# Optimization experiments

Measured on AMD Instinct MI355X. Metric: run time of the kernel, lower is better.

Reference implementation:

```python
import jax, jax.numpy as jnp
import numpy as np

B, S, H = 4, 1024, 1024
NH, HD = 16, 64
SCALE = 1.0 / np.sqrt(HD)
VERB_BIAS, ROOT_BIAS, SUFFIX_BIAS = 2.0, 1.5, 1.2
BIG = np.float32(1e9)


def setup_inputs() -> dict:
    key = jax.random.key(0)
    ks = jax.random.split(key, 10)
    inp = {
        "hidden_states": jax.random.normal(ks[0], (B, S, H), dtype=jnp.float32),
        "morpho_types": jax.random.randint(ks[1], (B, S), 0, 5, dtype=jnp.int32),
        # torch Linear: y = x @ W.T + b; store W already transposed as [in, out]
        "Wq": jax.random.normal(ks[2], (H, H), dtype=jnp.float32) * 0.02,
        "bq": jnp.zeros((H,), dtype=jnp.float32),
        "Wk": jax.random.normal(ks[3], (H, H), dtype=jnp.float32) * 0.02,
        "bk": jnp.zeros((H,), dtype=jnp.float32),
        "Wv": jax.random.normal(ks[4], (H, H), dtype=jnp.float32) * 0.02,
        "bv": jnp.zeros((H,), dtype=jnp.float32),
        "Wo": jax.random.normal(ks[5], (H, H), dtype=jnp.float32) * 0.02,
        "bo": jnp.zeros((H,), dtype=jnp.float32),
    }
    return inp


def _morpho_bias(morpho_types):
    """Vectorized equivalent of _create_morpho_bias_mask. Returns [B, S, S]
    (the torch version broadcasts the same bias over all heads)."""
    is_verb = morpho_types == 2                      # [B, S]
    pos = jnp.arange(S)
    dist = jnp.abs(pos[:, None] - pos[None, :])      # [S, S]
    # mask non-verb columns with a huge distance; argmin ties -> smallest j,
    # matching torch's argmin over ascending verb_positions
    dist_m = jnp.where(is_verb[:, None, :], dist[None], BIG)  # [B, S, S]
    nearest = jnp.argmin(dist_m, axis=-1)            # [B, S]
    has_verb = jnp.any(is_verb, axis=-1)             # [B]
    verb_term = VERB_BIAS * jax.nn.one_hot(nearest, S, dtype=jnp.float32)
    verb_term = verb_term * has_verb[:, None, None].astype(jnp.float32)
    col_bias = (ROOT_BIAS * 0.5) * (morpho_types == 0).astype(jnp.float32) \
             + (SUFFIX_BIAS * 0.3) * (morpho_types == 1).astype(jnp.float32)  # [B, S]
    return verb_term + col_bias[:, None, :]          # [B, S, S]


def reference(hidden_states, morpho_types, Wq, bq, Wk, bk, Wv, bv, Wo, bo):
    def proj(W, b):
        y = hidden_states @ W + b                    # [B, S, H]
        return y.reshape(B, S, NH, HD).transpose(0, 2, 1, 3)  # [B, NH, S, HD]

    q = proj(Wq, bq)
    k = proj(Wk, bk)
    v = proj(Wv, bv)

    scores = jnp.einsum('bhqd,bhkd->bhqk', q, k) * SCALE   # [B, NH, S, S]
    scores = scores + _morpho_bias(morpho_types)[:, None]  # broadcast heads

    attn = jax.nn.softmax(scores, axis=-1)
    out = jnp.einsum('bhqk,bhkd->bhqd', attn, v)           # [B, NH, S, HD]
    out = out.transpose(0, 2, 1, 3).reshape(B, S, H)
    return out @ Wo + bo
```

## Files before the change

kernel.cpp:

```cpp
#include <hip/hip_runtime.h>


#define QSCALE 0.18033688011112042f
#define CB0    1.0820212806667225f
#define CB1    0.5193702147200268f
#define VERB2  2.8853900817779268f

typedef float  f32x4   __attribute__((ext_vector_type(4)));
typedef short  s16x8   __attribute__((ext_vector_type(8)));
typedef unsigned short u16x4 __attribute__((ext_vector_type(4)));
typedef unsigned short u16x8 __attribute__((ext_vector_type(8)));

#if __has_builtin(__builtin_amdgcn_exp2f)
#define EXP2F(x) __builtin_amdgcn_exp2f(x)
#else
#define EXP2F(x) exp2f(x)
#endif

__device__ __forceinline__ unsigned short f2bf(float f) {
  union { float f; unsigned u; } a; a.f = f;
  unsigned r = a.u + 0x7fffu + ((a.u >> 16) & 1u);
  return (unsigned short)(r >> 16);
}

__device__ __forceinline__ void async16(const void* g, void* l) {
  __builtin_amdgcn_global_load_lds(
      (const __attribute__((address_space(1))) unsigned int*)g,
      (__attribute__((address_space(3))) unsigned int*)l, 16, 0, 0);
}

__global__ __launch_bounds__(256) void k_prep(
    const float* __restrict__ hs, unsigned short* __restrict__ hsb,
    const float* __restrict__ Wq, const float* __restrict__ Wk,
    const float* __restrict__ Wv, const float* __restrict__ Wo,
    unsigned short* __restrict__ Wt, const int* __restrict__ mt,
    float* __restrict__ colbias, int* __restrict__ nearest) {
  __shared__ float t[64 * 68];
  int bx = blockIdx.x, tid = threadIdx.x;
  if (bx < 2048) {
    int i = (bx * 256 + tid) * 8;
    float4 v0 = *(const float4*)(hs + i);
    float4 v1 = *(const float4*)(hs + i + 4);
    u16x8 o;
    o[0] = f2bf(v0.x); o[1] = f2bf(v0.y); o[2] = f2bf(v0.z); o[3] = f2bf(v0.w);
    o[4] = f2bf(v1.x); o[5] = f2bf(v1.y); o[6] = f2bf(v1.z); o[7] = f2bf(v1.w);
    *(u16x8*)(hsb + i) = o;
  } else if (bx < 3072) {
    int w = (bx - 2048) >> 8, tt = (bx - 2048) & 255;
    const float* W = (w == 0) ? Wq : (w == 1) ? Wk : (w == 2) ? Wv : Wo;
    unsigned short* Wd = Wt + (size_t)w * 1048576;
    int n0 = (tt & 15) * 64, k0 = (tt >> 4) * 64;
    int r = tid >> 2, c0 = (tid & 3) * 16;
    const float* src = &W[(k0 + r) * 1024 + n0 + c0];
    float4 a0 = *(const float4*)(src + 0);
    float4 a1 = *(const float4*)(src + 4);
    float4 a2 = *(const float4*)(src + 8);
    float4 a3 = *(const float4*)(src + 12);
    *(float4*)&t[r * 68 + c0 + 0]  = a0;
    *(float4*)&t[r * 68 + c0 + 4]  = a1;
    *(float4*)&t[r * 68 + c0 + 8]  = a2;
    *(float4*)&t[r * 68 + c0 + 12] = a3;
    __syncthreads();
    u16x8 o0, o1;
#pragma unroll
    for (int j = 0; j < 8; j++) {
      o0[j] = f2bf(t[(c0 + j) * 68 + r]);
      o1[j] = f2bf(t[(c0 + 8 + j) * 68 + r]);
    }
    *(u16x8*)&Wd[(n0 + r) * 1024 + k0 + c0]     = o0;
    *(u16x8*)&Wd[(n0 + r) * 1024 + k0 + c0 + 8] = o1;
  } else {
    int i = bx - 3072;
    int b = i >> 2;
    int* sm = (int*)t;
    for (int j = tid; j < 1024; j += 256) sm[j] = mt[b * 1024 + j];
    __syncthreads();
    int q = (i & 3) * 256 + tid;
    int best = 1 << 30, bj = -1;
    for (int j = 0; j < 1024; ++j) {
      int d = (q > j) ? (q - j) : (j - q);
      int dd = (sm[j] == 2) ? d : (1 << 30);
      if (dd < best) { best = dd; bj = j; }
    }
    nearest[b * 1024 + q] = bj;
    int m = sm[q];
    colbias[b * 1024 + q] = CB0 * (m == 0) + CB1 * (m == 1);
  }
}

template <int MODE>
__global__ __launch_bounds__(256) void k_gemm(
    const unsigned short* __restrict__ A,
    const unsigned short* __restrict__ WtBase,
    const float* __restrict__ bias0, const float* __restrict__ bias1,
    const float* __restrict__ bias2,
    unsigned short* __restrict__ outB, unsigned short* __restrict__ outV,
    float* __restrict__ outF) {
  __shared__ unsigned short As[128 * 32];
  __shared__ unsigned short Bs[128 * 32];
  int tid = threadIdx.x, wid = tid >> 6, lane = tid & 63;
  int c = lane & 15, quad = lane >> 4;
  int m0, wsel, n0;
  const unsigned short* Bt;
  const float* bias;
  if (MODE == 0) {
    int lin = blockIdx.x + 24 * blockIdx.y;
    int xcd = lin & 7, idx = lin >> 3;
    m0 = (((xcd >> 1) << 3) + (idx & 7)) * 128;
    int xt = (xcd & 1) * 12 + (idx >> 3);
    wsel = xt >> 3;
    n0 = (xt & 7) * 128;
    Bt = WtBase + wsel * 1048576;
    bias = (wsel == 0) ? bias0 : ((wsel == 1) ? bias1 : bias2);
  } else {
    int lin = blockIdx.x + 8 * blockIdx.y;
    int xcd = lin & 7, idx = lin >> 3;
    m0 = ((xcd << 2) + (idx & 3)) * 128;
    n0 = (idx >> 2) * 128;
    wsel = 0; Bt = WtBase; bias = bias0;
  }
  int wm = (wid >> 1) * 64, wn = (wid & 1) * 64;
  const unsigned short* ga = A  + (m0 + wid * 32 + (lane >> 2)) * 1024 + (lane & 3) * 8;
  const unsigned short* gb = Bt + (n0 + wid * 32 + (lane >> 2)) * 1024 + (lane & 3) * 8;
  unsigned short* lA = &As[wid * 32 * 32];
  unsigned short* lB = &Bs[wid * 32 * 32];

  f32x4 acc[4][4];
#pragma unroll
  for (int i = 0; i < 4; i++)
#pragma unroll
    for (int j = 0; j < 4; j++) acc[i][j] = (f32x4){0.f, 0.f, 0.f, 0.f};

  bool sw = (MODE == 1) || (wsel != 2);

  for (int k0 = 0; k0 < 1024; k0 += 32) {
    async16(ga + k0,             lA);
    async16(ga + 16 * 1024 + k0, lA + 16 * 32);
    async16(gb + k0,             lB);
    async16(gb + 16 * 1024 + k0, lB + 16 * 32);
    __syncthreads();
    s16x8 af[4], bf[4];
#pragma unroll
    for (int i = 0; i < 4; i++) af[i] = *(const s16x8*)&As[(wm + i * 16 + c) * 32 + quad * 8];
#pragma unroll
    for (int j = 0; j < 4; j++) bf[j] = *(const s16x8*)&Bs[(wn + j * 16 + c) * 32 + quad * 8];
    if (sw) {
#pragma unroll
      for (int i = 0; i < 4; i++)
#pragma unroll
        for (int j = 0; j < 4; j++)
          acc[i][j] = __builtin_amdgcn_mfma_f32_16x16x32_bf16(bf[j], af[i], acc[i][j], 0, 0, 0);
    } else {
#pragma unroll
      for (int i = 0; i < 4; i++)
#pragma unroll
        for (int j = 0; j < 4; j++)
          acc[i][j] = __builtin_amdgcn_mfma_f32_16x16x32_bf16(af[i], bf[j], acc[i][j], 0, 0, 0);
    }
    __syncthreads();
  }

  if (MODE == 1) {
#pragma unroll
    for (int j = 0; j < 4; j++) {
      int colb = n0 + wn + j * 16 + quad * 4;
      f32x4 bvv = *(const f32x4*)&bias[colb];
#pragma unroll
      for (int i = 0; i < 4; i++) {
        int s_tok = m0 + wm + i * 16 + c;
        f32x4 v = acc[i][j] + bvv;
        *(f32x4*)&outF[(size_t)s_tok * 1024 + colb] = v;
      }
    }
  } else if (wsel == 2) {
#pragma unroll
    for (int j = 0; j < 4; j++) {
      int col = n0 + wn + j * 16 + c;
      float bv = bias[col];
      int h = col >> 6, d = col & 63;
#pragma unroll
      for (int i = 0; i < 4; i++) {
        int row = m0 + wm + i * 16 + quad * 4;
        int bb = row >> 10, s = row & 1023;
        u16x4 pk;
#pragma unroll
        for (int r = 0; r < 4; r++) pk[r] = f2bf(acc[i][j][r] + bv);
        *(u16x4*)&outV[(size_t)(((bb * 16 + h) * 64 + d)) * 1024 + s] = pk;
      }
    }
  } else {
    float sc = (wsel == 0) ? QSCALE : 1.0f;
#pragma unroll
    for (int j = 0; j < 4; j++) {
      int colb = n0 + wn + j * 16 + quad * 4;
      f32x4 bvv = *(const f32x4*)&bias[colb];
      int h = colb >> 6, d0 = colb & 63;
#pragma unroll
      for (int i = 0; i < 4; i++) {
        int s_tok = m0 + wm + i * 16 + c;
        int bb = s_tok >> 10, s = s_tok & 1023;
        u16x4 pk;
#pragma unroll
        for (int r = 0; r < 4; r++) pk[r] = f2bf((acc[i][j][r] + bvv[r]) * sc);
        *(u16x4*)&outB[(size_t)wsel * 4194304 + (((bb * 16 + h) * 1024 + s) * 64) + d0] = pk;
      }
    }
  }
}

__global__ __launch_bounds__(256) void k_attn(
    const unsigned short* __restrict__ Q, const unsigned short* __restrict__ K,
    const unsigned short* __restrict__ Vt, const float* __restrict__ colbias,
    const int* __restrict__ nearest, unsigned short* __restrict__ AO) {
  __shared__ unsigned short Ks[64 * 72];
  __shared__ unsigned short Vs[64 * 72];
  __shared__ unsigned short Ps[4][32 * 72];
  __shared__ float Cb[1024];
  int tid = threadIdx.x, wid = tid >> 6, lane = tid & 63;
  int c = lane & 15, quad = lane >> 4;
  int bh = blockIdx.x, qt = blockIdx.y;
  int b = bh >> 4, head = bh & 15;
  int q0 = qt * 128, wq = wid * 32;
  const unsigned short* Qg = Q  + (size_t)(bh * 1024 + q0 + wq) * 64;
  const unsigned short* Kg = K  + (size_t)bh * 1024 * 64;
  const unsigned short* Vg = Vt + (size_t)bh * 64 * 1024;

  *(float4*)&Cb[tid * 4] = *(const float4*)&colbias[b * 1024 + tid * 4];

  s16x8 qf[2][2];
#pragma unroll
  for (int nt = 0; nt < 2; nt++)
#pragma unroll
    for (int ks = 0; ks < 2; ks++)
      qf[nt][ks] = *(const s16x8*)&Qg[(nt * 16 + c) * 64 + ks * 32 + quad * 8];

  int nq[2];
  nq[0] = nearest[b * 1024 + q0 + wq + c];
  nq[1] = nearest[b * 1024 + q0 + wq + 16 + c];

  f32x4 o[2][4];
#pragma unroll
  for (int i = 0; i < 2; i++)
#pragma unroll
    for (int j = 0; j < 4; j++) o[i][j] = (f32x4){0.f, 0.f, 0.f, 0.f};
  float lrun[2] = {0.f, 0.f};

  int srow = tid >> 3, scol8 = (tid & 7) * 8;

  u16x8 kr[2], vr[2];
#pragma unroll
  for (int it = 0; it < 2; ++it) {
    int r2 = it * 32 + srow;
    kr[it] = *(const u16x8*)&Kg[r2 * 64 + scol8];
    vr[it] = *(const u16x8*)&Vg[r2 * 1024 + scol8];
  }
  __syncthreads();

  for (int kc = 0; kc < 16; ++kc) {
#pragma unroll
    for (int it = 0; it < 2; ++it) {
      int r2 = it * 32 + srow;
      *(u16x8*)&Ks[r2 * 72 + scol8] = kr[it];
      *(u16x8*)&Vs[r2 * 72 + scol8] = vr[it];
    }
    __syncthreads();
    if (kc < 15) {
#pragma unroll
      for (int it = 0; it < 2; ++it) {
        int r2 = it * 32 + srow;
        kr[it] = *(const u16x8*)&Kg[((kc + 1) * 64 + r2) * 64 + scol8];
        vr[it] = *(const u16x8*)&Vg[r2 * 1024 + (kc + 1) * 64 + scol8];
      }
    }

    f32x4 st[4][2];
#pragma unroll
    for (int mt = 0; mt < 4; mt++)
#pragma unroll
      for (int nt = 0; nt < 2; nt++) st[mt][nt] = (f32x4){0.f, 0.f, 0.f, 0.f};
#pragma unroll
    for (int mt = 0; mt < 4; mt++)
#pragma unroll
      for (int ks = 0; ks < 2; ks++) {
        s16x8 a = *(const s16x8*)&Ks[(mt * 16 + c) * 72 + ks * 32 + quad * 8];
#pragma unroll
        for (int nt = 0; nt < 2; nt++)
          st[mt][nt] = __builtin_amdgcn_mfma_f32_16x16x32_bf16(a, qf[nt][ks], st[mt][nt], 0, 0, 0);
      }

#pragma unroll
    for (int mt = 0; mt < 4; mt++) {
      f32x4 cb = *(const f32x4*)&Cb[kc * 64 + mt * 16 + quad * 4];
#pragma unroll
      for (int nt = 0; nt < 2; nt++) {
        u16x4 pk;
#pragma unroll
        for (int r = 0; r < 4; r++) {
          int keyg = kc * 64 + mt * 16 + quad * 4 + r;
          float x = st[mt][nt][r] + cb[r] + ((keyg == nq[nt]) ? VERB2 : 0.f);
          float e = EXP2F(x);
          lrun[nt] += e;
          pk[r] = f2bf(e);
        }
        *(u16x4*)&Ps[wid][(nt * 16 + c) * 72 + mt * 16 + quad * 4] = pk;
      }
    }
    __asm__ volatile("s_waitcnt lgkmcnt(0)" ::: "memory");

#pragma unroll
    for (int ks = 0; ks < 2; ks++) {
      s16x8 pa[2];
#pragma unroll
      for (int mtq = 0; mtq < 2; mtq++)
        pa[mtq] = *(const s16x8*)&Ps[wid][(mtq * 16 + c) * 72 + ks * 32 + quad * 8];
#pragma unroll
      for (int ntd = 0; ntd < 4; ntd++) {
        s16x8 vb = *(const s16x8*)&Vs[(ntd * 16 + c) * 72 + ks * 32 + quad * 8];
#pragma unroll
        for (int mtq = 0; mtq < 2; mtq++)
          o[mtq][ntd] = __builtin_amdgcn_mfma_f32_16x16x32_bf16(vb, pa[mtq], o[mtq][ntd], 0, 0, 0);
      }
    }
    __syncthreads();
  }

#pragma unroll
  for (int nt = 0; nt < 2; nt++) {
    lrun[nt] += __shfl_xor(lrun[nt], 16, 64);
    lrun[nt] += __shfl_xor(lrun[nt], 32, 64);
  }
  float linv[2] = {1.0f / lrun[0], 1.0f / lrun[1]};
#pragma unroll
  for (int mtq = 0; mtq < 2; mtq++) {
    size_t row = (size_t)(b * 1024 + q0 + wq + mtq * 16 + c);
#pragma unroll
    for (int ntd = 0; ntd < 4; ntd++) {
      int d0 = ntd * 16 + quad * 4;
      u16x4 pk;
#pragma unroll
      for (int r = 0; r < 4; r++) pk[r] = f2bf(o[mtq][ntd][r] * linv[mtq]);
      *(u16x4*)&AO[row * 1024 + head * 64 + d0] = pk;
    }
  }
}

extern "C" void kernel_launch(void* const* d_in, const int* in_sizes, int n_in,
                              void* d_out, int out_size, void* d_ws, size_t ws_size,
                              hipStream_t stream) {
  const float* hs     = (const float*)d_in[0];
  const int*   morpho = (const int*)d_in[1];
  const float* Wq = (const float*)d_in[2];
  const float* bq = (const float*)d_in[3];
  const float* Wk = (const float*)d_in[4];
  const float* bk = (const float*)d_in[5];
  const float* Wv = (const float*)d_in[6];
  const float* bv = (const float*)d_in[7];
  const float* Wo = (const float*)d_in[8];
  const float* bo = (const float*)d_in[9];
  float* out = (float*)d_out;

  char* ws = (char*)d_ws;
  unsigned short* hsb = (unsigned short*)(ws);
  unsigned short* Wt  = (unsigned short*)(ws + (8u << 20));
  unsigned short* Qb  = (unsigned short*)(ws + (16u << 20));
  unsigned short* Kb  = (unsigned short*)(ws + (24u << 20));
  unsigned short* Vtb = (unsigned short*)(ws + (40u << 20));
  float* colbias      = (float*)(ws + (48u << 20));
  int*   nearestp     = (int*)(ws + (48u << 20) + (16u << 10));
  unsigned short* AO  = hsb;

  k_prep<<<3088, 256, 0, stream>>>(hs, hsb, Wq, Wk, Wv, Wo, Wt, morpho,
                                   colbias, nearestp);
  k_gemm<0><<<dim3(24, 32), 256, 0, stream>>>(hsb, Wt, bq, bk, bv, Qb, Vtb, nullptr);
  k_attn<<<dim3(64, 8), 256, 0, stream>>>(Qb, Kb, Vtb, colbias, nearestp, AO);
  k_gemm<1><<<dim3(8, 32), 256, 0, stream>>>(AO, Wt + 3 * 1048576, bo, nullptr, nullptr,
                                             nullptr, nullptr, out);
  (void)in_sizes; (void)n_in; (void)out_size; (void)ws_size; (void)Kb;
}
```

Before: 229.8 us.

## Double-buffer LDS tiles in the projection GEMM to overlap loads with MFMA

```diff
diff --git a/kernel.cpp b/kernel.cpp
--- a/kernel.cpp
+++ b/kernel.cpp
@@ -96,8 +96,8 @@
     const float* __restrict__ bias2,
     unsigned short* __restrict__ outB, unsigned short* __restrict__ outV,
     float* __restrict__ outF) {
-  __shared__ unsigned short As[128 * 32];
-  __shared__ unsigned short Bs[128 * 32];
+  __shared__ unsigned short As[2][128 * 32];
+  __shared__ unsigned short Bs[2][128 * 32];
   int tid = threadIdx.x, wid = tid >> 6, lane = tid & 63;
   int c = lane & 15, quad = lane >> 4;
   int m0, wsel, n0;
@@ -122,8 +122,7 @@
   int wm = (wid >> 1) * 64, wn = (wid & 1) * 64;
   const unsigned short* ga = A  + (m0 + wid * 32 + (lane >> 2)) * 1024 + (lane & 3) * 8;
   const unsigned short* gb = Bt + (n0 + wid * 32 + (lane >> 2)) * 1024 + (lane & 3) * 8;
-  unsigned short* lA = &As[wid * 32 * 32];
-  unsigned short* lB = &Bs[wid * 32 * 32];
+  int woff = wid * 32 * 32;
 
   f32x4 acc[4][4];
 #pragma unroll
@@ -133,17 +132,28 @@
 
   bool sw = (MODE == 1) || (wsel != 2);
 
+  async16(ga,             &As[0][woff]);
+  async16(ga + 16 * 1024, &As[0][woff + 16 * 32]);
+  async16(gb,             &Bs[0][woff]);
+  async16(gb + 16 * 1024, &Bs[0][woff + 16 * 32]);
+
   for (int k0 = 0; k0 < 1024; k0 += 32) {
-    async16(ga + k0,             lA);
-    async16(ga + 16 * 1024 + k0, lA + 16 * 32);
-    async16(gb + k0,             lB);
-    async16(gb + 16 * 1024 + k0, lB + 16 * 32);
-    __syncthreads();
+    int buf = (k0 >> 5) & 1;
+    __syncthreads();
+    if (k0 < 992) {
+      int nb = buf ^ 1, kn = k0 + 32;
+      async16(ga + kn,             &As[nb][woff]);
+      async16(ga + 16 * 1024 + kn, &As[nb][woff + 16 * 32]);
+      async16(gb + kn,             &Bs[nb][woff]);
+      async16(gb + 16 * 1024 + kn, &Bs[nb][woff + 16 * 32]);
+    }
     s16x8 af[4], bf[4];
 #pragma unroll
-    for (int i = 0; i < 4; i++) af[i] = *(const s16x8*)&As[(wm + i * 16 + c) * 32 + quad * 8];
-#pragma unroll
-    for (int j = 0; j < 4; j++) bf[j] = *(const s16x8*)&Bs[(wn + j * 16 + c) * 32 + quad * 8];
+    for (int i = 0; i < 4; i++)
+      af[i] = *(const s16x8*)&As[buf][(wm + i * 16 + c) * 32 + quad * 8];
+#pragma unroll
+    for (int j = 0; j < 4; j++)
+      bf[j] = *(const s16x8*)&Bs[buf][(wn + j * 16 + c) * 32 + quad * 8];
     if (sw) {
 #pragma unroll
       for (int i = 0; i < 4; i++)
@@ -157,7 +167,6 @@
         for (int j = 0; j < 4; j++)
           acc[i][j] = __builtin_amdgcn_mfma_f32_16x16x32_bf16(af[i], bf[j], acc[i][j], 0, 0, 0);
     }
-    __syncthreads();
   }
 
   if (MODE == 1) {
```

New measurement: 236.5 us. +2.9%, slower.

## Load GEMM fragments directly from global into registers with prefetch, drop LDS staging

Applied to the files above, without the earlier changes.

```diff
diff --git a/kernel.cpp b/kernel.cpp
--- a/kernel.cpp
+++ b/kernel.cpp
@@ -21,12 +21,6 @@
   union { float f; unsigned u; } a; a.f = f;
   unsigned r = a.u + 0x7fffu + ((a.u >> 16) & 1u);
   return (unsigned short)(r >> 16);
-}
-
-__device__ __forceinline__ void async16(const void* g, void* l) {
-  __builtin_amdgcn_global_load_lds(
-      (const __attribute__((address_space(1))) unsigned int*)g,
-      (__attribute__((address_space(3))) unsigned int*)l, 16, 0, 0);
 }
 
 __global__ __launch_bounds__(256) void k_prep(
@@ -89,15 +83,14 @@
 }
 
 template <int MODE>
-__global__ __launch_bounds__(256) void k_gemm(
+__global__ __launch_bounds__(256, 3) void k_gemm(
     const unsigned short* __restrict__ A,
     const unsigned short* __restrict__ WtBase,
     const float* __restrict__ bias0, const float* __restrict__ bias1,
     const float* __restrict__ bias2,
     unsigned short* __restrict__ outB, unsigned short* __restrict__ outV,
     float* __restrict__ outF) {
-  __shared__ unsigned short As[128 * 32];
-  __shared__ unsigned short Bs[128 * 32];
+  constexpr int NI = (MODE == 0) ? 4 : 2;
   int tid = threadIdx.x, wid = tid >> 6, lane = tid & 63;
   int c = lane & 15, quad = lane >> 4;
   int m0, wsel, n0;
@@ -115,49 +108,68 @@
   } else {
     int lin = blockIdx.x + 8 * blockIdx.y;
     int xcd = lin & 7, idx = lin >> 3;
-    m0 = ((xcd << 2) + (idx & 3)) * 128;
-    n0 = (idx >> 2) * 128;
+    m0 = ((xcd << 3) + (idx & 7)) * 64;
+    n0 = (idx >> 3) * 128;
     wsel = 0; Bt = WtBase; bias = bias0;
   }
-  int wm = (wid >> 1) * 64, wn = (wid & 1) * 64;
-  const unsigned short* ga = A  + (m0 + wid * 32 + (lane >> 2)) * 1024 + (lane & 3) * 8;
-  const unsigned short* gb = Bt + (n0 + wid * 32 + (lane >> 2)) * 1024 + (lane & 3) * 8;
-  unsigned short* lA = &As[wid * 32 * 32];
-  unsigned short* lB = &Bs[wid * 32 * 32];
-
-  f32x4 acc[4][4];
-#pragma unroll
-  for (int i = 0; i < 4; i++)
+  int wm = (wid >> 1) * (NI * 16), wn = (wid & 1) * 64;
+  const unsigned short* abase = A  + (size_t)(m0 + wm + c) * 1024 + quad * 8;
+  const unsigned short* bbase = Bt + (size_t)(n0 + wn + c) * 1024 + quad * 8;
+
+  f32x4 acc[NI][4];
+#pragma unroll
+  for (int i = 0; i < NI; i++)
 #pragma unroll
     for (int j = 0; j < 4; j++) acc[i][j] = (f32x4){0.f, 0.f, 0.f, 0.f};
 
   bool sw = (MODE == 1) || (wsel != 2);
 
-  for (int k0 = 0; k0 < 1024; k0 += 32) {
-    async16(ga + k0,             lA);
-    async16(ga + 16 * 1024 + k0, lA + 16 * 32);
-    async16(gb + k0,             lB);
-    async16(gb + 16 * 1024 + k0, lB + 16 * 32);
-    __syncthreads();
-    s16x8 af[4], bf[4];
-#pragma unroll
-    for (int i = 0; i < 4; i++) af[i] = *(const s16x8*)&As[(wm + i * 16 + c) * 32 + quad * 8];
-#pragma unroll
-    for (int j = 0; j < 4; j++) bf[j] = *(const s16x8*)&Bs[(wn + j * 16 + c) * 32 + quad * 8];
-    if (sw) {
-#pragma unroll
-      for (int i = 0; i < 4; i++)
+  s16x8 af[NI], bf[4];
+#pragma unroll
+  for (int i = 0; i < NI; i++) af[i] = *(const s16x8*)(abase + i * 16 * 1024);
+#pragma unroll
+  for (int j = 0; j < 4; j++)  bf[j] = *(const s16x8*)(bbase + j * 16 * 1024);
+
+  if (sw) {
+#pragma unroll 2
+    for (int k0 = 0; k0 < 1024; k0 += 32) {
+      s16x8 an[NI], bn[4];
+#pragma unroll
+      for (int i = 0; i < NI; i++)
+        an[i] = *(const s16x8*)(abase + k0 + 32 + i * 16 * 1024);
+#pragma unroll
+      for (int j = 0; j < 4; j++)
+        bn[j] = *(const s16x8*)(bbase + k0 + 32 + j * 16 * 1024);
+#pragma unroll
+      for (int i = 0; i < NI; i++)
 #pragma unroll
         for (int j = 0; j < 4; j++)
           acc[i][j] = __builtin_amdgcn_mfma_f32_16x16x32_bf16(bf[j], af[i], acc[i][j], 0, 0, 0);
-    } else {
-#pragma unroll
-      for (int i = 0; i < 4; i++)
+#pragma unroll
+      for (int i = 0; i < NI; i++) af[i] = an[i];
+#pragma unroll
+      for (int j = 0; j < 4; j++) bf[j] = bn[j];
+    }
+  } else {
+#pragma unroll 2
+    for (int k0 = 0; k0 < 1024; k0 += 32) {
+      s16x8 an[NI], bn[4];
+#pragma unroll
+      for (int i = 0; i < NI; i++)
+        an[i] = *(const s16x8*)(abase + k0 + 32 + i * 16 * 1024);
+#pragma unroll
+      for (int j = 0; j < 4; j++)
+        bn[j] = *(const s16x8*)(bbase + k0 + 32 + j * 16 * 1024);
+#pragma unroll
+      for (int i = 0; i < NI; i++)
 #pragma unroll
         for (int j = 0; j < 4; j++)
           acc[i][j] = __builtin_amdgcn_mfma_f32_16x16x32_bf16(af[i], bf[j], acc[i][j], 0, 0, 0);
-    }
-    __syncthreads();
+#pragma unroll
+      for (int i = 0; i < NI; i++) af[i] = an[i];
+#pragma unroll
+      for (int j = 0; j < 4; j++) bf[j] = bn[j];
+    }
   }
 
   if (MODE == 1) {
@@ -166,7 +178,7 @@
       int colb = n0 + wn + j * 16 + quad * 4;
       f32x4 bvv = *(const f32x4*)&bias[colb];
 #pragma unroll
-      for (int i = 0; i < 4; i++) {
+      for (int i = 0; i < NI; i++) {
         int s_tok = m0 + wm + i * 16 + c;
         f32x4 v = acc[i][j] + bvv;
         *(f32x4*)&outF[(size_t)s_tok * 1024 + colb] = v;
@@ -179,7 +191,7 @@
       float bv = bias[col];
       int h = col >> 6, d = col & 63;
 #pragma unroll
-      for (int i = 0; i < 4; i++) {
+      for (int i = 0; i < NI; i++) {
         int row = m0 + wm + i * 16 + quad * 4;
         int bb = row >> 10, s = row & 1023;
         u16x4 pk;
@@ -196,7 +208,7 @@
       f32x4 bvv = *(const f32x4*)&bias[colb];
       int h = colb >> 6, d0 = colb & 63;
 #pragma unroll
-      for (int i = 0; i < 4; i++) {
+      for (int i = 0; i < NI; i++) {
         int s_tok = m0 + wm + i * 16 + c;
         int bb = s_tok >> 10, s = s_tok & 1023;
         u16x4 pk;
@@ -373,7 +385,7 @@
                                    colbias, nearestp);
   k_gemm<0><<<dim3(24, 32), 256, 0, stream>>>(hsb, Wt, bq, bk, bv, Qb, Vtb, nullptr);
   k_attn<<<dim3(64, 8), 256, 0, stream>>>(Qb, Kb, Vtb, colbias, nearestp, AO);
-  k_gemm<1><<<dim3(8, 32), 256, 0, stream>>>(AO, Wt + 3 * 1048576, bo, nullptr, nullptr,
+  k_gemm<1><<<dim3(8, 64), 256, 0, stream>>>(AO, Wt + 3 * 1048576, bo, nullptr, nullptr,
                                              nullptr, nullptr, out);
   (void)in_sizes; (void)n_in; (void)out_size; (void)ws_size; (void)Kb;
 }
```

Result: slower. 297.7 us (+29.6%).
